# Performance work log

Measured on AMD Instinct MI355X. Metric: run time of the kernel, lower is better.

The kernel has to match this reference:

```python
import jax, jax.numpy as jnp
import numpy as np

B = 8192          # batch size
C = 512           # feature dim
NUM_CLASSES = 100
TOPK_POS = 8
TOPK_NEG = 64
TEMP = 0.5
EPS_NORM = 1e-12  # torch F.normalize eps


def setup_inputs() -> dict:
    key = jax.random.key(0)
    k1, k2, k3 = jax.random.split(key, 3)
    return {
        "old_feat": jax.random.normal(k1, (B, C), dtype=jnp.float32),
        "new_feat": jax.random.normal(k2, (B, C), dtype=jnp.float32),
        "target": jax.random.randint(k3, (B,), 0, NUM_CLASSES, dtype=jnp.int64),
    }


def _l2_normalize(x):
    n = jnp.sqrt(jnp.sum(x * x, axis=1, keepdims=True))
    return x / jnp.maximum(n, EPS_NORM)


def _cl_loss(new_feat, target):
    inf = jnp.inf
    nf = _l2_normalize(new_feat)                       # [B, C]
    sim = nf @ nf.T                                    # [B, B] cosine sims ('nn' pair)
    classwise = target[:, None] == target[None, :]     # [B, B] same-class mask

    # positives: smallest TOPK_POS sims among same-class entries (non-class -> +inf)
    sim_pos = jnp.where(classwise, sim, inf)
    pos = -jax.lax.top_k(-sim_pos, TOPK_POS)[0]        # [B, P] smallest-k

    # negatives: largest TOPK_NEG sims among other-class entries (same-class -> -inf)
    sim_neg = jnp.where(classwise, -inf, sim)
    neg = jax.lax.top_k(sim_neg, TOPK_NEG)[0]          # [B, K]

    # pair_all: [B, P, 1+K] -- each positive vs all mined negatives
    pair_all = jnp.concatenate(
        [pos[:, :, None], jnp.broadcast_to(neg[:, None, :], (B, TOPK_POS, TOPK_NEG))],
        axis=2,
    ) / TEMP
    # criterion: input[input == inf] = -inf
    x = jnp.where(jnp.isposinf(pair_all), -inf, pair_all)

    # multi-label CE with one-hot-at-column-0 targets -> -log_softmax[..., 0]
    logp = jax.nn.log_softmax(x, axis=-1)
    l = -logp[..., 0]                                  # [B, P]
    l = jnp.where(jnp.isfinite(l), l, 0.0)             # zero out inf/nan rows
    return l.mean(axis=1)                              # [B]


def reference(old_feat, new_feat, target):
    # pair = {pos: 'nn', neg: 'nn'} -> only new_feat similarities used;
    # old_feat participates in the signature (and would be used for 'on'/'oo' pairs)
    return _cl_loss(new_feat, target)
```

## Files before the change

### kernel.cpp

```cpp
#include <hip/hip_runtime.h>
#include <hip/hip_bf16.h>

#define B_N 8192
#define C_DIM 512
#define NT 64
#define NTRI 2080
#define TGKEY 0xBDC0u

typedef __attribute__((ext_vector_type(4))) float f32x4;
typedef __attribute__((ext_vector_type(4))) int i32x4;
typedef __attribute__((address_space(3))) unsigned int lds_u32;
typedef const __attribute__((address_space(1))) unsigned int glb_u32;

__device__ __forceinline__ void gl_lds16b(const unsigned char* g, unsigned char* l) {
    __builtin_amdgcn_global_load_lds((glb_u32*)g, (lds_u32*)l, 16, 0, 0);
}

__device__ __forceinline__ unsigned short f2bf(float f) {
    unsigned int u = __float_as_uint(f);
    u += 0x7FFFu + ((u >> 16) & 1u);
    return (unsigned short)(u >> 16);
}
__device__ __forceinline__ float bf2f(unsigned int s) {
    return __uint_as_float(s << 16);
}
__device__ __forceinline__ unsigned negkey(unsigned ub) {
    return (ub & 0x8000u) ? ((~ub) & 0xFFFFu) : (ub | 0x8000u);
}
__device__ __forceinline__ unsigned unkey(unsigned k) {
    return (k & 0x8000u) ? (k ^ 0x8000u) : ((~k) & 0xFFFFu);
}

__global__ void prep_all(const unsigned int* __restrict__ t, unsigned char* __restrict__ tgb,
                         unsigned short* __restrict__ clist, int* __restrict__ off) {
    __shared__ int bad, cnt[128], base[128];
    const int tid = threadIdx.x;
    if (tid == 0) bad = 0;
    if (tid < 128) cnt[tid] = 0;
    __syncthreads();
    int local = 0;
    for (int k = tid; k < 4096; k += 256)
        if (t[2 * k + 1] != 0u) local = 1;
    if (local) atomicOr(&bad, 1);
    __syncthreads();
    const int is64 = (bad == 0);
    for (int i = 0; i < 32; ++i) {
        int j = i * 256 + tid;
        unsigned c = (is64 ? t[2 * j] : t[j]) & 127u;
        tgb[j] = (unsigned char)c;
        atomicAdd(&cnt[c], 1);
    }
    __syncthreads();
    if (tid == 0) {
        int s = 0;
        for (int c = 0; c < 128; ++c) { base[c] = s; off[c] = s; s += cnt[c]; }
        off[128] = s;
    }
    __syncthreads();
    for (int i = 0; i < 32; ++i) {
        int j = i * 256 + tid;
        unsigned c = (is64 ? t[2 * j] : t[j]) & 127u;
        int idx = atomicAdd(&base[c], 1);
        clist[idx] = (unsigned short)j;
    }
}

__global__ void class_masks(const unsigned char* __restrict__ tgb,
                            unsigned int* __restrict__ cm2) {
    const int c = blockIdx.x, t = threadIdx.x;
    unsigned w = 0;
#pragma unroll
    for (int q = 0; q < 4; ++q) {
        const unsigned char* base = tgb + q * 2048 + t * 8;
        unsigned b = 0;
#pragma unroll
        for (int e = 0; e < 8; ++e)
            b |= ((unsigned)(base[e] == c)) << e;
        w |= b << (8 * q);
    }
    cm2[c * 256 + t] = w;
}

__global__ __launch_bounds__(256) void normalize_k(const float* __restrict__ x,
                                                   unsigned char* __restrict__ nf8) {
    const int wid = threadIdx.x >> 6, lane = threadIdx.x & 63;
    const size_t row = (size_t)blockIdx.x * 4 + wid;
    const float4* xr = (const float4*)(x + row * C_DIM) + lane * 2;
    float4 a = xr[0], b = xr[1];
    float ss = a.x * a.x + a.y * a.y + a.z * a.z + a.w * a.w +
               b.x * b.x + b.y * b.y + b.z * b.z + b.w * b.w;
#pragma unroll
    for (int m = 1; m < 64; m <<= 1) ss += __shfl_xor(ss, m);
    float sc = 1.0f / fmaxf(sqrtf(ss), 1e-12f);
    int w0 = __builtin_amdgcn_cvt_pk_fp8_f32(a.x * sc, a.y * sc, 0, false);
    w0 = __builtin_amdgcn_cvt_pk_fp8_f32(a.z * sc, a.w * sc, w0, true);
    int w1 = __builtin_amdgcn_cvt_pk_fp8_f32(b.x * sc, b.y * sc, 0, false);
    w1 = __builtin_amdgcn_cvt_pk_fp8_f32(b.z * sc, b.w * sc, w1, true);
    int2 o2; o2.x = w0; o2.y = w1;
    *(int2*)(nf8 + row * C_DIM + lane * 8) = o2;
}

__global__ __launch_bounds__(256) void gemm_sim(const unsigned char* __restrict__ nf8,
                                                unsigned short* __restrict__ simk,
                                                int rowBase, int symmetric) {
    __shared__ __align__(16) unsigned char smemB[34816];
    unsigned char* As8 = smemB;
    unsigned char* Bs8 = smemB + 16384;
    int tI, tJ;
    if (symmetric) {
        const int idp = (NTRI - 1) - (int)blockIdx.x;
        int u = (int)((sqrtf(8.0f * (float)idp + 1.0f) - 1.0f) * 0.5f);
        while (u * (u + 1) / 2 > idp) --u;
        while ((u + 1) * (u + 2) / 2 <= idp) ++u;
        const int v = idp - u * (u + 1) / 2;
        tI = (NT - 1) - u;
        tJ = (NT - 1) - v;
    } else {
        tI = blockIdx.y; tJ = blockIdx.x;
    }
    const int tid = threadIdx.x;
    const int wid = tid >> 6, lane = tid & 63;
    const int wm = wid >> 1, wn = wid & 1;
    const int gr = rowBase + tI * 128;
    const int gc = tJ * 128;
    f32x4 zero = {0.f, 0.f, 0.f, 0.f};
    f32x4 acc[4][4];
#pragma unroll
    for (int m = 0; m < 4; ++m)
#pragma unroll
        for (int n = 0; n < 4; ++n) acc[m][n] = zero;

    const int lr = lane >> 3, lcb = lane & 7;

    for (int k0 = 0; k0 < C_DIM; k0 += 128) {
#pragma unroll
        for (int i = 0; i < 4; ++i) {
            const int chunk = wid * 4 + i;
            const int r = chunk * 8 + lr;
            const int sc = (lcb ^ (r & 7)) << 4;
            gl_lds16b(nf8 + (size_t)(gr + r) * C_DIM + k0 + sc, As8 + chunk * 1024);
            gl_lds16b(nf8 + (size_t)(gc + r) * C_DIM + k0 + sc, Bs8 + chunk * 1024);
        }
        __syncthreads();
#pragma unroll
        for (int kk = 0; kk < 4; ++kk) {
            const int krow = kk * 32 + (lane >> 4) * 8;
            long a[4], b[4];
#pragma unroll
            for (int m = 0; m < 4; ++m) {
                const int R = wm * 64 + m * 16 + (lane & 15);
                a[m] = *(const long*)&As8[R * 128 + (krow ^ ((R & 7) << 4))];
            }
#pragma unroll
            for (int n = 0; n < 4; ++n) {
                const int R = wn * 64 + n * 16 + (lane & 15);
                b[n] = *(const long*)&Bs8[R * 128 + (krow ^ ((R & 7) << 4))];
            }
#pragma unroll
            for (int m = 0; m < 4; ++m)
#pragma unroll
                for (int n = 0; n < 4; ++n)
                    acc[m][n] = __builtin_amdgcn_mfma_f32_16x16x32_fp8_fp8(a[m], b[n], acc[m][n], 0, 0, 0);
        }
        __syncthreads();
    }

    unsigned short kk4[4][4][4];
#pragma unroll
    for (int m = 0; m < 4; ++m)
#pragma unroll
        for (int n = 0; n < 4; ++n)
#pragma unroll
            for (int j = 0; j < 4; ++j)
                kk4[m][n][j] = (unsigned short)negkey(f2bf(acc[m][n][j]));

    unsigned short* Cs = (unsigned short*)smemB;
    const int fc = (lane & 15);
    const int fr = (lane >> 4) << 2;

#pragma unroll
    for (int m = 0; m < 4; ++m)
#pragma unroll
        for (int n = 0; n < 4; ++n) {
            const int c = wn * 64 + n * 16 + fc;
            const int r0 = wm * 64 + m * 16 + fr;
#pragma unroll
            for (int j = 0; j < 4; ++j)
                Cs[(r0 + j) * 136 + c] = kk4[m][n][j];
        }
    __syncthreads();
#pragma unroll
    for (int k = 0; k < 8; ++k) {
        const int lin = tid + k * 256;
        const int r = lin >> 4;
        const int c0 = (lin & 15) * 8;
        i32x4 v = *(const i32x4*)&Cs[r * 136 + c0];
        __builtin_nontemporal_store(v, (i32x4*)&simk[(size_t)(gr - rowBase + r) * B_N + gc + c0]);
    }

    if (symmetric && tJ > tI) {
        __syncthreads();
#pragma unroll
        for (int m = 0; m < 4; ++m)
#pragma unroll
            for (int n = 0; n < 4; ++n) {
                const int c = wn * 64 + n * 16 + fc;
                const int r0 = wm * 64 + m * 16 + fr;
                ushort4 pk;
                pk.x = kk4[m][n][0]; pk.y = kk4[m][n][1];
                pk.z = kk4[m][n][2]; pk.w = kk4[m][n][3];
                *(ushort4*)&Cs[c * 136 + r0] = pk;
            }
        __syncthreads();
#pragma unroll
        for (int k = 0; k < 8; ++k) {
            const int lin = tid + k * 256;
            const int c = lin >> 4;
            const int r0 = (lin & 15) * 8;
            i32x4 v = *(const i32x4*)&Cs[c * 136 + r0];
            __builtin_nontemporal_store(v, (i32x4*)&simk[(size_t)(gc + c) * B_N + gr + r0]);
        }
    }
}

__global__ __launch_bounds__(256) void select_loss(const unsigned short* __restrict__ simk,
                                                   const unsigned char* __restrict__ tgb,
                                                   const unsigned int* __restrict__ cm2,
                                                   const unsigned short* __restrict__ clist,
                                                   const int* __restrict__ off,
                                                   float* __restrict__ out, int rowBase) {
    __shared__ int nlist[256];
    __shared__ float s_partial[4];
    __shared__ int nln, s_cnt;

    const int tid = threadIdx.x;
    const int wid = tid >> 6, lane = tid & 63;
    const int row = rowBase + blockIdx.x;
    const unsigned short* srow = simk + (size_t)blockIdx.x * B_N;
    const int ti = tgb[row];
    const int o0 = off[ti], o1 = off[ti + 1];

    int4 A[4];
    const unsigned m = cm2[ti * 256 + tid];
#pragma unroll
    for (int q = 0; q < 4; ++q) {
        A[q] = *(const int4*)(srow + q * 2048 + tid * 8);
#pragma unroll
        for (int d = 0; d < 4; ++d) {
            unsigned two = (m >> (q * 8 + d * 2)) & 3u;
            unsigned kill = ((two & 1u) * 0xFFFFu) | (((two >> 1) & 1u) * 0xFFFF0000u);
            int v = (d == 0 ? A[q].x : d == 1 ? A[q].y : d == 2 ? A[q].z : A[q].w);
            v = (int)((unsigned)v & ~kill);
            if (d == 0) A[q].x = v; else if (d == 1) A[q].y = v;
            else if (d == 2) A[q].z = v; else A[q].w = v;
        }
    }
    if (tid == 0) { nln = 0; s_cnt = 0; }
    __syncthreads();

#define ELEM_LOOP(BODY)                                                          \
    _Pragma("unroll")                                                            \
    for (int q = 0; q < 4; ++q) {                                                \
        _Pragma("unroll")                                                        \
        for (int d = 0; d < 4; ++d) {                                            \
            unsigned w32 = (unsigned)(d == 0 ? A[q].x : d == 1 ? A[q].y          \
                                    : d == 2 ? A[q].z : A[q].w);                 \
            _Pragma("unroll")                                                    \
            for (int h2 = 0; h2 < 2; ++h2) {                                     \
                unsigned key = h2 ? (w32 >> 16) : (w32 & 0xFFFFu);               \
                BODY                                                             \
            }                                                                    \
        }                                                                        \
    }

    ELEM_LOOP(
        if (key > TGKEY) { int p = atomicAdd(&nln, 1); if (p < 256) nlist[p] = (int)key; }
    )
    __syncthreads();
    const int NC = nln;

    unsigned thr;
    int kremf;
    float S;

    if (NC >= 64 && NC <= 256) {
        if (wid != 0) return;
        unsigned pk[8];
#pragma unroll
        for (int s2 = 0; s2 < 8; ++s2) {
            int idx = o0 + lane + s2 * 64;
            pk[s2] = (idx < o1)
                ? ((((unsigned)srow[clist[idx]]) << 9) | ((unsigned)lane << 3) | (unsigned)s2)
                : 0xFFFFFFFFu;
        }
        int4 cw = *(const int4*)&nlist[lane * 4];
        unsigned cand[4] = {(unsigned)cw.x, (unsigned)cw.y, (unsigned)cw.z, (unsigned)cw.w};
#pragma unroll
        for (int j = 0; j < 4; ++j)
            if (lane * 4 + j >= NC) cand[j] = 0;
        unsigned cur = 0;
#pragma unroll
        for (int bit = 15; bit >= 0; --bit) {
            unsigned trial = cur | (1u << bit);
            int c = (cand[0] >= trial) + (cand[1] >= trial) +
                    (cand[2] >= trial) + (cand[3] >= trial);
#pragma unroll
            for (int o = 1; o < 64; o <<= 1) c += __shfl_xor(c, o);
            if (c >= 64) cur = trial;
        }
        int r = (cand[0] > cur) + (cand[1] > cur) + (cand[2] > cur) + (cand[3] > cur);
#pragma unroll
        for (int o = 1; o < 64; o <<= 1) r += __shfl_xor(r, o);
        kremf = 64 - r;
        float f = 0.f;
#pragma unroll
        for (int j = 0; j < 4; ++j)
            if (cand[j] > cur) f += __expf(2.0f * bf2f(unkey(cand[j])));
#pragma unroll
        for (int o = 1; o < 64; o <<= 1) f += __shfl_xor(f, o);
        S = f;
        thr = cur;

        S += (float)kremf * __expf(2.0f * bf2f(unkey(thr)));
        float acc = 0.f;
#pragma unroll
        for (int rd = 0; rd < 8; ++rd) {
            unsigned best = pk[0];
#pragma unroll
            for (int s2 = 1; s2 < 8; ++s2) best = best < pk[s2] ? best : pk[s2];
#pragma unroll
            for (int o = 1; o < 64; o <<= 1) {
                unsigned v = (unsigned)__shfl_xor((int)best, o);
                best = best < v ? best : v;
            }
            if (best != 0xFFFFFFFFu) {
                if (lane == (int)((best >> 3) & 63u)) pk[best & 7u] = 0xFFFFFFFFu;
                if (lane == 0) {
                    float p = bf2f(unkey(best >> 9));
                    acc += logf(__expf(2.0f * p) + S) - 2.0f * p;
                }
            }
        }
        if (lane == 0) out[row] = acc * 0.125f;
    } else {
        unsigned cur = 0;
        for (int bit = 15; bit >= 0; --bit) {
            unsigned trial = cur | (1u << bit);
            int c = 0;
            ELEM_LOOP( c += (key >= trial) ? 1 : 0; )
#pragma unroll
            for (int o = 1; o < 64; o <<= 1) c += __shfl_xor(c, o);
            if (lane == 0) atomicAdd(&s_cnt, c);
            __syncthreads();
            int tot = s_cnt;
            __syncthreads();
            if (tid == 0) s_cnt = 0;
            __syncthreads();
            if (tot >= 64) cur = trial;
        }
        {
            int c = 0;
            ELEM_LOOP( c += (key > cur) ? 1 : 0; )
#pragma unroll
            for (int o = 1; o < 64; o <<= 1) c += __shfl_xor(c, o);
            if (lane == 0) atomicAdd(&s_cnt, c);
            __syncthreads();
        }
        const int r = s_cnt;
        kremf = 64 - r;
        {
            float f = 0.f;
            ELEM_LOOP( if (key > cur) f += __expf(2.0f * bf2f(unkey(key))); )
#pragma unroll
            for (int o = 1; o < 64; o <<= 1) f += __shfl_xor(f, o);
            if (lane == 0) s_partial[wid] = f;
            __syncthreads();
        }
        if (wid != 0) return;
        S = s_partial[0] + s_partial[1] + s_partial[2] + s_partial[3];
        thr = cur;

        unsigned pk[8];
#pragma unroll
        for (int s2 = 0; s2 < 8; ++s2) {
            int idx = o0 + lane + s2 * 64;
            pk[s2] = (idx < o1)
                ? ((((unsigned)srow[clist[idx]]) << 9) | ((unsigned)lane << 3) | (unsigned)s2)
                : 0xFFFFFFFFu;
        }
        S += (float)kremf * __expf(2.0f * bf2f(unkey(thr)));
        float acc = 0.f;
#pragma unroll
        for (int rd = 0; rd < 8; ++rd) {
            unsigned best = pk[0];
#pragma unroll
            for (int s2 = 1; s2 < 8; ++s2) best = best < pk[s2] ? best : pk[s2];
#pragma unroll
            for (int o = 1; o < 64; o <<= 1) {
                unsigned v = (unsigned)__shfl_xor((int)best, o);
                best = best < v ? best : v;
            }
            if (best != 0xFFFFFFFFu) {
                if (lane == (int)((best >> 3) & 63u)) pk[best & 7u] = 0xFFFFFFFFu;
                if (lane == 0) {
                    float p = bf2f(unkey(best >> 9));
                    acc += logf(__expf(2.0f * p) + S) - 2.0f * p;
                }
            }
        }
        if (lane == 0) out[row] = acc * 0.125f;
    }
#undef ELEM_LOOP
}

extern "C" void kernel_launch(void* const* d_in, const int* in_sizes, int n_in,
                              void* d_out, int out_size, void* d_ws, size_t ws_size,
                              hipStream_t stream) {
    const float* newf = (const float*)d_in[1];
    const unsigned int* tgtw = (const unsigned int*)d_in[2];
    float* out = (float*)d_out;
    char* ws = (char*)d_ws;
    unsigned char* tgb = (unsigned char*)ws;
    unsigned int* cm2 = (unsigned int*)(ws + 8192);
    int* off = (int*)(ws + 110592);
    unsigned short* clist = (unsigned short*)(ws + 111616);
    unsigned char* nf8 = (unsigned char*)(ws + 131072);
    unsigned short* simk = (unsigned short*)(ws + 131072 + ((size_t)4 << 20));

    size_t fixed = 131072 + ((size_t)4 << 20);
    size_t avail = (ws_size > fixed) ? (ws_size - fixed) : 0;
    long maxRows = (long)(avail / ((size_t)B_N * 2));
    int chunk = (int)((maxRows / 128) * 128);
    if (chunk < 128) chunk = 128;
    if (chunk > B_N) chunk = B_N;

    hipLaunchKernelGGL(prep_all, dim3(1), dim3(256), 0, stream, tgtw, tgb, clist, off);
    hipLaunchKernelGGL(class_masks, dim3(100), dim3(256), 0, stream, tgb, cm2);
    hipLaunchKernelGGL(normalize_k, dim3(B_N / 4), dim3(256), 0, stream, newf, nf8);
    if (chunk == B_N) {
        hipLaunchKernelGGL(gemm_sim, dim3(NTRI), dim3(256), 0, stream, nf8, simk, 0, 1);
        hipLaunchKernelGGL(select_loss, dim3(B_N), dim3(256), 0, stream,
                           simk, tgb, cm2, clist, off, out, 0);
    } else {
        for (int r0 = 0; r0 < B_N; r0 += chunk) {
            int rows = (B_N - r0 < chunk) ? (B_N - r0) : chunk;
            hipLaunchKernelGGL(gemm_sim, dim3(64, rows / 128), dim3(256), 0, stream,
                               nf8, simk, r0, 0);
            hipLaunchKernelGGL(select_loss, dim3(rows), dim3(256), 0, stream,
                               simk, tgb, cm2, clist, off, out, r0);
        }
    }
}
```

Measured before the change: 122.9 us.

## Add 256x256 double-buffered symmetric GEMM kernel for full similarity matrix

Adds a new symmetric similarity GEMM that uses 256x256 output tiles with 512 threads, computing only the upper triangle (528 tiles) and mirroring results. The K loop is double-buffered with 64-wide K stages so global-to-LDS loads overlap with MFMA work. The larger tiles halve operand reloads per output element but need 64KB of LDS and more accumulator registers, which may reduce occupancy. The epilogue writes four quadrants in sequence through LDS, which adds more barriers.

Result: slower. 145.1 us (+18.0%).

```diff
diff --git a/kernel.cpp b/kernel.cpp
--- a/kernel.cpp
+++ b/kernel.cpp
@@ -5,6 +5,8 @@
 #define C_DIM 512
 #define NT 64
 #define NTRI 2080
+#define NT2 32
+#define NTRI2 528
 #define TGKEY 0xBDC0u
 
 typedef __attribute__((ext_vector_type(4))) float f32x4;
@@ -100,24 +102,160 @@
     *(int2*)(nf8 + row * C_DIM + lane * 8) = o2;
 }
 
+__global__ __launch_bounds__(512, 2) void gemm_sim256(const unsigned char* __restrict__ nf8,
+                                                      unsigned short* __restrict__ simk) {
+    __shared__ __align__(16) unsigned char smem[2][32768];
+    const int idp = (NTRI2 - 1) - (int)blockIdx.x;
+    int u = (int)((sqrtf(8.0f * (float)idp + 1.0f) - 1.0f) * 0.5f);
+    while (u * (u + 1) / 2 > idp) --u;
+    while ((u + 1) * (u + 2) / 2 <= idp) ++u;
+    const int v = idp - u * (u + 1) / 2;
+    const int tI = (NT2 - 1) - u;
+    const int tJ = (NT2 - 1) - v;
+
+    const int tid = threadIdx.x;
+    const int wid = tid >> 6, lane = tid & 63;
+    const int wm = wid >> 2, wn = wid & 3;
+    const int gr = tI * 256, gc = tJ * 256;
+    f32x4 zero = {0.f, 0.f, 0.f, 0.f};
+    f32x4 acc[8][4];
+#pragma unroll
+    for (int m = 0; m < 8; ++m)
+#pragma unroll
+        for (int n = 0; n < 4; ++n) acc[m][n] = zero;
+
+    const int slr = lane >> 2;
+    const int slg = lane & 3;
+
+#define STAGE(b, k0)                                                              \
+    {                                                                             \
+        _Pragma("unroll")                                                         \
+        for (int i = 0; i < 2; ++i) {                                             \
+            const int chunk = wid * 2 + i;                                        \
+            const int r = chunk * 16 + slr;                                       \
+            const int sc = (slg ^ ((r >> 1) & 3)) << 4;                           \
+            gl_lds16b(nf8 + (size_t)(gr + r) * C_DIM + (k0) + sc,                 \
+                      &smem[b][chunk * 1024]);                                    \
+            gl_lds16b(nf8 + (size_t)(gc + r) * C_DIM + (k0) + sc,                 \
+                      &smem[b][16384 + chunk * 1024]);                            \
+        }                                                                         \
+    }
+
+    STAGE(0, 0)
+    __syncthreads();
+    int cur = 0;
+    for (int t = 0; t < 8; ++t) {
+        if (t + 1 < 8) STAGE(cur ^ 1, (t + 1) * 64)
+        const unsigned char* As8 = &smem[cur][0];
+        const unsigned char* Bs8 = &smem[cur][16384];
+#pragma unroll
+        for (int kk = 0; kk < 2; ++kk) {
+            const int krow = kk * 32 + (lane >> 4) * 8;
+            long a[8], b[4];
+#pragma unroll
+            for (int m = 0; m < 8; ++m) {
+                const int R = wm * 128 + m * 16 + (lane & 15);
+                a[m] = *(const long*)&As8[R * 64 + (krow ^ (((R >> 1) & 3) << 4))];
+            }
+#pragma unroll
+            for (int n = 0; n < 4; ++n) {
+                const int R = wn * 64 + n * 16 + (lane & 15);
+                b[n] = *(const long*)&Bs8[R * 64 + (krow ^ (((R >> 1) & 3) << 4))];
+            }
+#pragma unroll
+            for (int m = 0; m < 8; ++m)
+#pragma unroll
+                for (int n = 0; n < 4; ++n)
+                    acc[m][n] = __builtin_amdgcn_mfma_f32_16x16x32_fp8_fp8(a[m], b[n], acc[m][n], 0, 0, 0);
+        }
+        __syncthreads();
+        cur ^= 1;
+    }
+#undef STAGE
+
+    unsigned short kk8[8][4][4];
+#pragma unroll
+    for (int m = 0; m < 8; ++m)
+#pragma unroll
+        for (int n = 0; n < 4; ++n)
+#pragma unroll
+            for (int j = 0; j < 4; ++j)
+                kk8[m][n][j] = (unsigned short)negkey(f2bf(acc[m][n][j]));
+
+    unsigned short* Cs = (unsigned short*)&smem[0][0];
+    const int fc = lane & 15;
+    const int fr = (lane >> 4) << 2;
+    const bool mirror = (tJ > tI);
+
+#pragma unroll
+    for (int qm = 0; qm < 2; ++qm)
+#pragma unroll
+        for (int qn = 0; qn < 2; ++qn) {
+            __syncthreads();
+            if (wm == qm && (wn >> 1) == qn) {
+#pragma unroll
+                for (int m = 0; m < 8; ++m)
+#pragma unroll
+                    for (int n = 0; n < 4; ++n) {
+                        const int rl = m * 16 + fr;
+                        const int cl = (wn & 1) * 64 + n * 16 + fc;
+#pragma unroll
+                        for (int j = 0; j < 4; ++j)
+                            Cs[(rl + j) * 136 + cl] = kk8[m][n][j];
+                    }
+            }
+            __syncthreads();
+#pragma unroll
+            for (int k = 0; k < 4; ++k) {
+                const int lin = tid + k * 512;
+                const int r = lin >> 4;
+                const int c0 = (lin & 15) * 8;
+                i32x4 vv = *(const i32x4*)&Cs[r * 136 + c0];
+                __builtin_nontemporal_store(vv,
+                    (i32x4*)&simk[(size_t)(gr + qm * 128 + r) * B_N + gc + qn * 128 + c0]);
+            }
+        }
+
+    if (mirror) {
+#pragma unroll
+        for (int qm = 0; qm < 2; ++qm)
+#pragma unroll
+            for (int qn = 0; qn < 2; ++qn) {
+                __syncthreads();
+                if (wm == qm && (wn >> 1) == qn) {
+#pragma unroll
+                    for (int m = 0; m < 8; ++m)
+#pragma unroll
+                        for (int n = 0; n < 4; ++n) {
+                            const int rl = m * 16 + fr;
+                            const int cl = (wn & 1) * 64 + n * 16 + fc;
+                            ushort4 pk;
+                            pk.x = kk8[m][n][0]; pk.y = kk8[m][n][1];
+                            pk.z = kk8[m][n][2]; pk.w = kk8[m][n][3];
+                            *(ushort4*)&Cs[cl * 136 + rl] = pk;
+                        }
+                }
+                __syncthreads();
+#pragma unroll
+                for (int k = 0; k < 4; ++k) {
+                    const int lin = tid + k * 512;
+                    const int c = lin >> 4;
+                    const int r0 = (lin & 15) * 8;
+                    i32x4 vv = *(const i32x4*)&Cs[c * 136 + r0];
+                    __builtin_nontemporal_store(vv,
+                        (i32x4*)&simk[(size_t)(gc + qn * 128 + c) * B_N + gr + qm * 128 + r0]);
+                }
+            }
+    }
+}
+
 __global__ __launch_bounds__(256) void gemm_sim(const unsigned char* __restrict__ nf8,
                                                 unsigned short* __restrict__ simk,
-                                                int rowBase, int symmetric) {
+                                                int rowBase) {
     __shared__ __align__(16) unsigned char smemB[34816];
     unsigned char* As8 = smemB;
     unsigned char* Bs8 = smemB + 16384;
-    int tI, tJ;
-    if (symmetric) {
-        const int idp = (NTRI - 1) - (int)blockIdx.x;
-        int u = (int)((sqrtf(8.0f * (float)idp + 1.0f) - 1.0f) * 0.5f);
-        while (u * (u + 1) / 2 > idp) --u;
-        while ((u + 1) * (u + 2) / 2 <= idp) ++u;
-        const int v = idp - u * (u + 1) / 2;
-        tI = (NT - 1) - u;
-        tJ = (NT - 1) - v;
-    } else {
-        tI = blockIdx.y; tJ = blockIdx.x;
-    }
+    const int tI = blockIdx.y, tJ = blockIdx.x;
     const int tid = threadIdx.x;
     const int wid = tid >> 6, lane = tid & 63;
     const int wm = wid >> 1, wn = wid & 1;
@@ -129,9 +267,7 @@
     for (int m = 0; m < 4; ++m)
 #pragma unroll
         for (int n = 0; n < 4; ++n) acc[m][n] = zero;
-
     const int lr = lane >> 3, lcb = lane & 7;
-
     for (int k0 = 0; k0 < C_DIM; k0 += 128) {
 #pragma unroll
         for (int i = 0; i < 4; ++i) {
@@ -164,7 +300,6 @@
         }
         __syncthreads();
     }
-
     unsigned short kk4[4][4][4];
 #pragma unroll
     for (int m = 0; m < 4; ++m)
@@ -173,11 +308,9 @@
 #pragma unroll
             for (int j = 0; j < 4; ++j)
                 kk4[m][n][j] = (unsigned short)negkey(f2bf(acc[m][n][j]));
-
     unsigned short* Cs = (unsigned short*)smemB;
     const int fc = (lane & 15);
     const int fr = (lane >> 4) << 2;
-
 #pragma unroll
     for (int m = 0; m < 4; ++m)
 #pragma unroll
@@ -196,30 +329,6 @@
         const int c0 = (lin & 15) * 8;
         i32x4 v = *(const i32x4*)&Cs[r * 136 + c0];
         __builtin_nontemporal_store(v, (i32x4*)&simk[(size_t)(gr - rowBase + r) * B_N + gc + c0]);
-    }
-
-    if (symmetric && tJ > tI) {
-        __syncthreads();
-#pragma unroll
-        for (int m = 0; m < 4; ++m)
-#pragma unroll
-            for (int n = 0; n < 4; ++n) {
-                const int c = wn * 64 + n * 16 + fc;
-                const int r0 = wm * 64 + m * 16 + fr;
-                ushort4 pk;
-                pk.x = kk4[m][n][0]; pk.y = kk4[m][n][1];
-                pk.z = kk4[m][n][2]; pk.w = kk4[m][n][3];
-                *(ushort4*)&Cs[c * 136 + r0] = pk;
-            }
-        __syncthreads();
-#pragma unroll
-        for (int k = 0; k < 8; ++k) {
-            const int lin = tid + k * 256;
-            const int c = lin >> 4;
-            const int r0 = (lin & 15) * 8;
-            i32x4 v = *(const i32x4*)&Cs[c * 136 + r0];
-            __builtin_nontemporal_store(v, (i32x4*)&simk[(size_t)(gc + c) * B_N + gr + r0]);
-        }
     }
 }
 
@@ -438,14 +547,14 @@
     hipLaunchKernelGGL(class_masks, dim3(100), dim3(256), 0, stream, tgb, cm2);
     hipLaunchKernelGGL(normalize_k, dim3(B_N / 4), dim3(256), 0, stream, newf, nf8);
     if (chunk == B_N) {
-        hipLaunchKernelGGL(gemm_sim, dim3(NTRI), dim3(256), 0, stream, nf8, simk, 0, 1);
+        hipLaunchKernelGGL(gemm_sim256, dim3(NTRI2), dim3(512), 0, stream, nf8, simk);
         hipLaunchKernelGGL(select_loss, dim3(B_N), dim3(256), 0, stream,
                            simk, tgb, cm2, clist, off, out, 0);
     } else {
         for (int r0 = 0; r0 < B_N; r0 += chunk) {
             int rows = (B_N - r0 < chunk) ? (B_N - r0) : chunk;
-            hipLaunchKernelGGL(gemm_sim, dim3(64, rows / 128), dim3(256), 0, stream,
-                               nf8, simk, r0, 0);
+            hipLaunchKernelGGL(gemm_sim, dim3(NT, rows / 128), dim3(256), 0, stream,
+                               nf8, simk, r0);
             hipLaunchKernelGGL(select_loss, dim3(rows), dim3(256), 0, stream,
                                simk, tgb, cm2, clist, off, out, r0);
         }
```

## Double-buffer fp8 GEMM LDS tiles with K=64 stages to overlap loads

Applied to the files above, without the earlier changes.

The similarity GEMM now splits K into 8 stages of 64 bytes and double-buffers the A/B tiles in the existing 32 KB of LDS. It issues the global-to-LDS load for the next stage before running MFMAs on the current one. The swizzle changes to fit 64-byte rows. The aim is to hide global load latency behind compute, at the cost of twice as many barriers and smaller per-stage work.

Result: no change. 121.0 us (-1.6%).

```diff
diff --git a/kernel.cpp b/kernel.cpp
--- a/kernel.cpp
+++ b/kernel.cpp
@@ -104,8 +104,6 @@
                                                 unsigned short* __restrict__ simk,
                                                 int rowBase, int symmetric) {
     __shared__ __align__(16) unsigned char smemB[34816];
-    unsigned char* As8 = smemB;
-    unsigned char* Bs8 = smemB + 16384;
     int tI, tJ;
     if (symmetric) {
         const int idp = (NTRI - 1) - (int)blockIdx.x;
@@ -130,31 +128,43 @@
 #pragma unroll
         for (int n = 0; n < 4; ++n) acc[m][n] = zero;
 
-    const int lr = lane >> 3, lcb = lane & 7;
-
-    for (int k0 = 0; k0 < C_DIM; k0 += 128) {
-#pragma unroll
-        for (int i = 0; i < 4; ++i) {
-            const int chunk = wid * 4 + i;
-            const int r = chunk * 8 + lr;
-            const int sc = (lcb ^ (r & 7)) << 4;
-            gl_lds16b(nf8 + (size_t)(gr + r) * C_DIM + k0 + sc, As8 + chunk * 1024);
-            gl_lds16b(nf8 + (size_t)(gc + r) * C_DIM + k0 + sc, Bs8 + chunk * 1024);
-        }
-        __syncthreads();
-#pragma unroll
-        for (int kk = 0; kk < 4; ++kk) {
+    const int slr = lane >> 2;
+    const int slg = lane & 3;
+
+#define STAGE(b, k0)                                                              \
+    {                                                                             \
+        _Pragma("unroll")                                                         \
+        for (int i = 0; i < 2; ++i) {                                             \
+            const int chunk = wid * 2 + i;                \
+            const int r = chunk * 16 + slr;                                       \
+            const int sc = (slg ^ ((r >> 1) & 3)) << 4;                           \
+            gl_lds16b(nf8 + (size_t)(gr + r) * C_DIM + (k0) + sc,                 \
+                      smemB + (b) * 16384 + chunk * 1024);                        \
+            gl_lds16b(nf8 + (size_t)(gc + r) * C_DIM + (k0) + sc,                 \
+                      smemB + (b) * 16384 + 8192 + chunk * 1024);                 \
+        }                                                                         \
+    }
+
+    STAGE(0, 0)
+    __syncthreads();
+    int cur = 0;
+    for (int t = 0; t < 8; ++t) {
+        if (t + 1 < 8) STAGE(cur ^ 1, (t + 1) * 64)
+        const unsigned char* As8 = smemB + cur * 16384;
+        const unsigned char* Bs8 = As8 + 8192;
+#pragma unroll
+        for (int kk = 0; kk < 2; ++kk) {
             const int krow = kk * 32 + (lane >> 4) * 8;
             long a[4], b[4];
 #pragma unroll
             for (int m = 0; m < 4; ++m) {
                 const int R = wm * 64 + m * 16 + (lane & 15);
-                a[m] = *(const long*)&As8[R * 128 + (krow ^ ((R & 7) << 4))];
+                a[m] = *(const long*)&As8[R * 64 + (krow ^ (((R >> 1) & 3) << 4))];
             }
 #pragma unroll
             for (int n = 0; n < 4; ++n) {
                 const int R = wn * 64 + n * 16 + (lane & 15);
-                b[n] = *(const long*)&Bs8[R * 128 + (krow ^ ((R & 7) << 4))];
+                b[n] = *(const long*)&Bs8[R * 64 + (krow ^ (((R >> 1) & 3) << 4))];
             }
 #pragma unroll
             for (int m = 0; m < 4; ++m)
@@ -163,7 +173,9 @@
                     acc[m][n] = __builtin_amdgcn_mfma_f32_16x16x32_fp8_fp8(a[m], b[n], acc[m][n], 0, 0, 0);
         }
         __syncthreads();
-    }
+        cur ^= 1;
+    }
+#undef STAGE
 
     unsigned short kk4[4][4][4];
 #pragma unroll
@@ -444,7 +456,7 @@
     } else {
         for (int r0 = 0; r0 < B_N; r0 += chunk) {
             int rows = (B_N - r0 < chunk) ? (B_N - r0) : chunk;
-            hipLaunchKernelGGL(gemm_sim, dim3(64, rows / 128), dim3(256), 0, stream,
+            hipLaunchKernelGGL(gemm_sim, dim3(NT, rows / 128), dim3(256), 0, stream,
                                nf8, simk, r0, 0);
             hipLaunchKernelGGL(select_loss, dim3(rows), dim3(256), 0, stream,
                                simk, tgb, cm2, clist, off, out, r0);
```
